# Kernel tuning notes

Hardware: AMD Instinct MI355X
Metric: run time of the kernel (lower is better)

## Reference

```python
import jax, jax.numpy as jnp
import numpy as np

# dims: L layers, D d_model, H heads, DH head_dim, DFF ffn, V vocab, BLK nf4 blocksize
L, D, H, DH, DFF, V, BLK = 2, 2048, 16, 128, 5504, 32000, 64
B, S, C, T = 4, 1000, 7, 45

# bitsandbytes NF4 codebook (fixed 16 quantiles of N(0,1), normalized to [-1,1])
NF4 = jnp.array([-1.0, -0.6961928009986877, -0.5250730514526367, -0.39491748809814453,
                 -0.28444138169288635, -0.18477343022823334, -0.09105003625154495, 0.0,
                 0.07958029955625534, 0.16093020141124725, 0.24611230194568634,
                 0.3379152417182922, 0.44070982933044434, 0.5626170039176941,
                 0.7229568362236023, 1.0], dtype=jnp.float32)


def _dequant(idx, scale):
    # idx: [out, in] int in [0,16); scale: [out, in//BLK] per-block absmax
    o, i = idx.shape
    return (NF4[idx].reshape(o, i // BLK, BLK) * scale[:, :, None]).reshape(o, i)


def _rmsnorm(h, w, eps=1e-5):
    return h * jax.lax.rsqrt(jnp.mean(h * h, axis=-1, keepdims=True) + eps) * w


def _rot_half(x):
    x1, x2 = jnp.split(x, 2, axis=-1)
    return jnp.concatenate([-x2, x1], axis=-1)


def _llama_fwd(token_ids, embed, wq_idx, wq_scale, wk_idx, wk_scale, wv_idx, wv_scale,
               wo_idx, wo_scale, wg_idx, wg_scale, wu_idx, wu_scale, wd_idx, wd_scale,
               ln1_w, ln2_w, lnf_w):
    Bt, St = token_ids.shape
    h = embed[token_ids]  # [B,S,D]
    # rotary embeddings
    inv = 1.0 / (10000.0 ** (jnp.arange(0, DH, 2, dtype=jnp.float32) / DH))
    ang = jnp.arange(St, dtype=jnp.float32)[:, None] * inv[None, :]  # [S, DH/2]
    emb_ang = jnp.concatenate([ang, ang], axis=-1)  # [S, DH]
    cos, sin = jnp.cos(emb_ang), jnp.sin(emb_ang)
    mask = jnp.where(jnp.tril(jnp.ones((St, St), dtype=bool)), 0.0, -1e9)  # causal
    for l in range(L):
        xn = _rmsnorm(h, ln1_w[l])
        q = (xn @ _dequant(wq_idx[l], wq_scale[l]).T).reshape(Bt, St, H, DH).transpose(0, 2, 1, 3)
        k = (xn @ _dequant(wk_idx[l], wk_scale[l]).T).reshape(Bt, St, H, DH).transpose(0, 2, 1, 3)
        v = (xn @ _dequant(wv_idx[l], wv_scale[l]).T).reshape(Bt, St, H, DH).transpose(0, 2, 1, 3)
        q = q * cos + _rot_half(q) * sin
        k = k * cos + _rot_half(k) * sin
        att = jax.nn.softmax(jnp.einsum('bhqd,bhkd->bhqk', q, k) / np.float32(np.sqrt(DH)) + mask, axis=-1)
        ctx = jnp.einsum('bhqk,bhkd->bhqd', att, v).transpose(0, 2, 1, 3).reshape(Bt, St, D)
        h = h + ctx @ _dequant(wo_idx[l], wo_scale[l]).T
        xn = _rmsnorm(h, ln2_w[l])
        g = xn @ _dequant(wg_idx[l], wg_scale[l]).T
        u = xn @ _dequant(wu_idx[l], wu_scale[l]).T
        h = h + (jax.nn.silu(g) * u) @ _dequant(wd_idx[l], wd_scale[l]).T
    # hidden_states[-1].mean(dim=1)
    return _rmsnorm(h, lnf_w).mean(axis=1)


def setup_inputs() -> dict:
    key = jax.random.key(0)
    ks = jax.random.split(key, 20)
    ridx = lambda k, shp: jax.random.randint(k, shp, 0, 16, dtype=jnp.int32)
    rsc = lambda k, shp: jax.random.uniform(k, shp, minval=0.01, maxval=0.03, dtype=jnp.float32)
    return {
        'x': jax.random.normal(ks[0], (B, C, T), dtype=jnp.float32),
        'token_ids': jax.random.randint(ks[1], (B, S), 0, V, dtype=jnp.int32),
        'embed': jax.random.normal(ks[2], (V, D), dtype=jnp.float32) * 0.02,
        'wq_idx': ridx(ks[3], (L, D, D)), 'wq_scale': rsc(ks[4], (L, D, D // BLK)),
        'wk_idx': ridx(ks[5], (L, D, D)), 'wk_scale': rsc(ks[6], (L, D, D // BLK)),
        'wv_idx': ridx(ks[7], (L, D, D)), 'wv_scale': rsc(ks[8], (L, D, D // BLK)),
        'wo_idx': ridx(ks[9], (L, D, D)), 'wo_scale': rsc(ks[10], (L, D, D // BLK)),
        'wg_idx': ridx(ks[11], (L, DFF, D)), 'wg_scale': rsc(ks[12], (L, DFF, D // BLK)),
        'wu_idx': ridx(ks[13], (L, DFF, D)), 'wu_scale': rsc(ks[14], (L, DFF, D // BLK)),
        'wd_idx': ridx(ks[15], (L, D, DFF)), 'wd_scale': rsc(ks[16], (L, D, DFF // BLK)),
        'ln1_w': jnp.ones((L, D), dtype=jnp.float32),
        'ln2_w': jnp.ones((L, D), dtype=jnp.float32),
        'lnf_w': jnp.ones((D,), dtype=jnp.float32),
        'proj_w': jax.random.normal(ks[17], (D, T), dtype=jnp.float32) * 0.05,
        'proj_b': jnp.zeros((D,), dtype=jnp.float32),
    }


def reference(x, token_ids, embed, wq_idx, wq_scale, wk_idx, wk_scale, wv_idx, wv_scale,
              wo_idx, wo_scale, wg_idx, wg_scale, wu_idx, wu_scale, wd_idx, wd_scale,
              ln1_w, ln2_w, lnf_w, proj_w, proj_b):
    # NF4-quantized Llama-style causal LM forward + mean pool over sequence
    e_text = _llama_fwd(token_ids, embed, wq_idx, wq_scale, wk_idx, wk_scale, wv_idx, wv_scale,
                        wo_idx, wo_scale, wg_idx, wg_scale, wu_idx, wu_scale, wd_idx, wd_scale,
                        ln1_w, ln2_w, lnf_w)  # [B, D]
    # series branch: channel-mean -> linear -> L2 normalize
    series_mean = x.mean(axis=1)  # [B, T]
    series_emb = series_mean @ proj_w.T + proj_b  # [B, D]
    series_emb = series_emb / jnp.maximum(jnp.linalg.norm(series_emb, axis=-1, keepdims=True), 1e-12)
    return e_text + series_emb
```

## Files before the change

### kernel.cpp

```cpp
#include <hip/hip_runtime.h>
#include <hip/hip_bf16.h>

#define L_N 2
#define D_ 2048
#define H_ 16
#define DH_ 128
#define DFF_ 5504
#define B_ 4
#define S_ 1000
#define C_ 7
#define T_ 45
#define M_ 4000

typedef short bf16x8 __attribute__((ext_vector_type(8)));
typedef float f32x4 __attribute__((ext_vector_type(4)));

__constant__ float NF4_TAB[16] = {
  -1.0f, -0.6961928009986877f, -0.5250730514526367f, -0.39491748809814453f,
  -0.28444138169288635f, -0.18477343022823334f, -0.09105003625154495f, 0.0f,
  0.07958029955625534f, 0.16093020141124725f, 0.24611230194568634f,
  0.3379152417182922f, 0.44070982933044434f, 0.5626170039176941f,
  0.7229568362236023f, 1.0f };

__device__ __forceinline__ unsigned short f2bf(float f) {
  unsigned int u = __float_as_uint(f);
  u += 0x7fffu + ((u >> 16) & 1u);
  return (unsigned short)(u >> 16);
}
__device__ __forceinline__ float bf2f(unsigned short u) {
  return __uint_as_float(((unsigned int)u) << 16);
}
__device__ __forceinline__ f32x4 zero4() { f32x4 z; z[0]=0.f; z[1]=0.f; z[2]=0.f; z[3]=0.f; return z; }
__device__ __forceinline__ f32x4 mfma16(bf16x8 a, bf16x8 b, f32x4 c) {
  return __builtin_amdgcn_mfma_f32_16x16x32_bf16(a, b, c, 0, 0, 0);
}

typedef __attribute__((address_space(3))) unsigned int lds_u32;
typedef const __attribute__((address_space(1))) unsigned int glb_u32;
__device__ __forceinline__ void gload16(const void* g, void* l) {
  __builtin_amdgcn_global_load_lds((glb_u32*)g, (lds_u32*)l, 16, 0, 0);
}

__global__ void rope_tables(float* __restrict__ cosT, float* __restrict__ sinT) {
  int s = blockIdx.x, d = threadIdx.x;
  int j = d & 63;
  float inv = expf(-(float)j * (9.210340371976184f / 64.f));
  float ang = (float)s * inv;
  cosT[s * DH_ + d] = cosf(ang);
  sinT[s * DH_ + d] = sinf(ang);
}

__global__ __launch_bounds__(256) void embed_gather(const int* __restrict__ tok,
    const float* __restrict__ emb, float* __restrict__ h) {
  int row = blockIdx.x;
  int tk = tok[row];
  const float4* src = reinterpret_cast<const float4*>(emb + (size_t)tk * D_);
  float4* dst = reinterpret_cast<float4*>(h + (size_t)row * D_);
  dst[threadIdx.x] = src[threadIdx.x];
  dst[threadIdx.x + 256] = src[threadIdx.x + 256];
}

__global__ __launch_bounds__(256) void rmsnorm_k(float* __restrict__ h,
    const float* __restrict__ add, const float* __restrict__ w,
    unsigned short* __restrict__ out) {
  const int row = blockIdx.x, t = threadIdx.x;
  float* hp = h + (size_t)row * D_;
  float4 a = *reinterpret_cast<const float4*>(&hp[t * 8]);
  float4 b = *reinterpret_cast<const float4*>(&hp[t * 8 + 4]);
  if (add) {
    const float* ap = add + (size_t)row * D_;
    float4 da = *reinterpret_cast<const float4*>(&ap[t * 8]);
    float4 db = *reinterpret_cast<const float4*>(&ap[t * 8 + 4]);
    a.x += da.x; a.y += da.y; a.z += da.z; a.w += da.w;
    b.x += db.x; b.y += db.y; b.z += db.z; b.w += db.w;
    *reinterpret_cast<float4*>(&hp[t * 8]) = a;
    *reinterpret_cast<float4*>(&hp[t * 8 + 4]) = b;
  }
  float ss = a.x*a.x + a.y*a.y + a.z*a.z + a.w*a.w
           + b.x*b.x + b.y*b.y + b.z*b.z + b.w*b.w;
#pragma unroll
  for (int m = 1; m < 64; m <<= 1) ss += __shfl_xor(ss, m);
  __shared__ float red[4];
  if ((t & 63) == 0) red[t >> 6] = ss;
  __syncthreads();
  float tot = red[0] + red[1] + red[2] + red[3];
  float rs = rsqrtf(tot * (1.0f / D_) + 1e-5f);
  float4 wa = *reinterpret_cast<const float4*>(&w[t * 8]);
  float4 wb = *reinterpret_cast<const float4*>(&w[t * 8 + 4]);
  unsigned r0 = (unsigned)f2bf(a.x*rs*wa.x) | ((unsigned)f2bf(a.y*rs*wa.y) << 16);
  unsigned r1 = (unsigned)f2bf(a.z*rs*wa.z) | ((unsigned)f2bf(a.w*rs*wa.w) << 16);
  unsigned r2 = (unsigned)f2bf(b.x*rs*wb.x) | ((unsigned)f2bf(b.y*rs*wb.y) << 16);
  unsigned r3 = (unsigned)f2bf(b.z*rs*wb.z) | ((unsigned)f2bf(b.w*rs*wb.w) << 16);
  int4 ov; ov.x = (int)r0; ov.y = (int)r1; ov.z = (int)r2; ov.w = (int)r3;
  *reinterpret_cast<int4*>(&out[(size_t)row * D_ + t * 8]) = ov;
}

struct DqJob { const int* idx; const float* sc; unsigned short* out; };
struct DqBatch { DqJob j[4]; };

__global__ __launch_bounds__(256) void dequant_batch(DqBatch bt, int K) {
  __shared__ float nf4[16];
  const int t = threadIdx.x;
  if (t < 16) nf4[t] = NF4_TAB[t];
  __syncthreads();
  const DqJob jb = bt.j[blockIdx.z];
  const int row = blockIdx.y;
  const int k0 = blockIdx.x * 2048 + t * 8;
  if (k0 >= K) return;
  const size_t base = (size_t)row * K + k0;
  int4 a = *reinterpret_cast<const int4*>(&jb.idx[base]);
  int4 b = *reinterpret_cast<const int4*>(&jb.idx[base + 4]);
  float s = jb.sc[(size_t)row * (K >> 6) + (k0 >> 6)];
  unsigned r0 = (unsigned)f2bf(nf4[a.x & 15] * s) | ((unsigned)f2bf(nf4[a.y & 15] * s) << 16);
  unsigned r1 = (unsigned)f2bf(nf4[a.z & 15] * s) | ((unsigned)f2bf(nf4[a.w & 15] * s) << 16);
  unsigned r2 = (unsigned)f2bf(nf4[b.x & 15] * s) | ((unsigned)f2bf(nf4[b.y & 15] * s) << 16);
  unsigned r3 = (unsigned)f2bf(nf4[b.z & 15] * s) | ((unsigned)f2bf(nf4[b.w & 15] * s) << 16);
  int4 ov; ov.x = (int)r0; ov.y = (int)r1; ov.z = (int)r2; ov.w = (int)r3;
  *reinterpret_cast<int4*>(&jb.out[base]) = ov;
}

template<int MODE>
__global__ __launch_bounds__(256, 4) void gemm_bf16(
    const unsigned short* __restrict__ A,
    const unsigned short* __restrict__ Bw,
    const unsigned short* __restrict__ Bw2,
    int Mdim, int N, int K, int nx, int ksplit,
    void* outp, void* outp2, float* dscr) {
  __shared__ unsigned short A_lds[128 * 64];
  __shared__ unsigned short B_lds[128 * 64];
  const int t = threadIdx.x;
  const int lane = t & 63, wid = t >> 6;
  const int z = blockIdx.z;

  const unsigned short* Bsrc = (MODE == 0 && z) ? Bw2 : Bw;
  void* osel = (MODE == 0 && z) ? outp2 : outp;

  const int bid = blockIdx.x;
  const int xcd = bid & 7, l = bid >> 3;
  const int m_blk = xcd * 4 + (l & 3);
  const int n_blk = l >> 2;
  const int n0 = n_blk * 128;
  const int m0 = m_blk * 128;

  const int wm = (wid >> 1) * 64, wn = (wid & 1) * 64;
  const int lr = lane & 15, lg = lane >> 4;
  const int lrow = lane >> 3;
  const int lslot = (((lane & 7) ^ lrow) << 4);
  const int rswz = (lr & 7) << 4;

  f32x4 acc[4][4];
#pragma unroll
  for (int i = 0; i < 4; ++i)
#pragma unroll
    for (int j = 0; j < 4; ++j) acc[i][j] = zero4();

  const int kT = K >> 6;
  const int ktlo = (MODE == 3) ? (z ? ksplit : 0) : 0;
  const int kthi = (MODE == 3) ? (z ? kT : ksplit) : kT;
  const size_t rowb = (size_t)(K * 2);

  for (int kt = ktlo; kt < kthi; ++kt) {
#pragma unroll
    for (int c0 = 0; c0 < 4; ++c0) {
      const int c = wid + 4 * c0;
      int gr = m0 + c * 8 + lrow;
      gr = gr < Mdim ? gr : Mdim - 1;
      gload16((const char*)A + (size_t)gr * rowb + kt * 128 + lslot,
              (char*)&A_lds[0] + c * 1024);
      const int nr = n0 + c * 8 + lrow;
      gload16((const char*)Bsrc + (size_t)nr * rowb + kt * 128 + lslot,
              (char*)&B_lds[0] + c * 1024);
    }
    __syncthreads();
#pragma unroll
    for (int ks = 0; ks < 2; ++ks) {
      bf16x8 af[4], bfr[4];
      const int cb = (ks * 64 + lg * 16) ^ rswz;
#pragma unroll
      for (int i = 0; i < 4; ++i) {
        af[i]  = *reinterpret_cast<const bf16x8*>(
                   (const char*)&A_lds[0] + (wm + i * 16 + lr) * 128 + cb);
        bfr[i] = *reinterpret_cast<const bf16x8*>(
                   (const char*)&B_lds[0] + (wn + i * 16 + lr) * 128 + cb);
      }
      __builtin_amdgcn_s_setprio(1);
#pragma unroll
      for (int mi = 0; mi < 4; ++mi)
#pragma unroll
        for (int ni = 0; ni < 4; ++ni)
          acc[mi][ni] = mfma16(af[mi], bfr[ni], acc[mi][ni]);
      __builtin_amdgcn_s_setprio(0);
    }
    __syncthreads();
  }

#pragma unroll
  for (int mi = 0; mi < 4; ++mi) {
#pragma unroll
    for (int r = 0; r < 4; ++r) {
      int gm = m0 + wm + mi * 16 + lg * 4 + r;
      if (gm >= Mdim) continue;
#pragma unroll
      for (int ni = 0; ni < 4; ++ni) {
        int gn = n0 + wn + ni * 16 + lr;
        float v = acc[mi][ni][r];
        if (MODE == 0) {
          ((unsigned short*)osel)[(size_t)gm * N + gn] = f2bf(v);
        } else if (MODE == 1) {
          const int which = gn >> 11;
          const int hh = (gn >> 7) & 15, dd = gn & 127;
          const int b = gm / S_, s = gm - b * S_;
          ((unsigned short*)outp)[
            (((size_t)which * (B_ * H_) + b * H_ + hh) * S_ + s) * DH_ + dd] = f2bf(v);
        } else {
          if (z == 0) ((float*)outp)[(size_t)gm * N + gn] += v;
          else        dscr[(size_t)gm * N + gn] = v;
        }
      }
    }
  }
}

__global__ __launch_bounds__(256) void silu_mul(unsigned short* __restrict__ g,
    const unsigned short* __restrict__ u) {
  const size_t i = ((size_t)blockIdx.x * 256 + threadIdx.x) * 8;
  int4 gv = *reinterpret_cast<const int4*>(&g[i]);
  int4 uv = *reinterpret_cast<const int4*>(&u[i]);
  const unsigned* gp = reinterpret_cast<const unsigned*>(&gv);
  const unsigned* up = reinterpret_cast<const unsigned*>(&uv);
  unsigned ov[4];
#pragma unroll
  for (int j = 0; j < 4; ++j) {
    float g0 = bf2f(gp[j] & 0xffffu), g1 = bf2f(gp[j] >> 16);
    float u0 = bf2f(up[j] & 0xffffu), u1 = bf2f(up[j] >> 16);
    float s0 = g0 / (1.f + __expf(-g0)) * u0;
    float s1 = g1 / (1.f + __expf(-g1)) * u1;
    ov[j] = (unsigned)f2bf(s0) | ((unsigned)f2bf(s1) << 16);
  }
  int4 o; o.x = (int)ov[0]; o.y = (int)ov[1]; o.z = (int)ov[2]; o.w = (int)ov[3];
  *reinterpret_cast<int4*>(&g[i]) = o;
}

__global__ __launch_bounds__(256) void rope_apply(unsigned short* __restrict__ qb,
    unsigned short* __restrict__ kb, const float* __restrict__ cosT,
    const float* __restrict__ sinT) {
  size_t i = (size_t)blockIdx.x * 256 + threadIdx.x;
  int d = (int)(i & 63);
  size_t row = i >> 6;
  int s = (int)(row % S_);
  size_t base = row * DH_;
  float c = cosT[s * DH_ + d], sn = sinT[s * DH_ + d];
  float q0 = bf2f(qb[base + d]), q1 = bf2f(qb[base + d + 64]);
  qb[base + d]      = f2bf(q0 * c - q1 * sn);
  qb[base + d + 64] = f2bf(q1 * c + q0 * sn);
  float k0 = bf2f(kb[base + d]), k1 = bf2f(kb[base + d + 64]);
  kb[base + d]      = f2bf(k0 * c - k1 * sn);
  kb[base + d + 64] = f2bf(k1 * c + k0 * sn);
}

__global__ __launch_bounds__(256) void vtrans_k(const unsigned short* __restrict__ vb,
    unsigned short* __restrict__ vt) {
  __shared__ unsigned int tile[64][33];
  const int t = threadIdx.x;
  const int s0 = blockIdx.x * 64, d0 = blockIdx.y * 64, bh = blockIdx.z;
#pragma unroll
  for (int j = 0; j < 2; ++j) {
    int idx = t + 256 * j;
    int s_r = idx >> 3, c8 = (idx & 7) << 3;
    int srow = s0 + s_r; srow = srow < S_ ? srow : S_ - 1;
    int4 v = *reinterpret_cast<const int4*>(&vb[((size_t)bh * S_ + srow) * DH_ + d0 + c8]);
    tile[s_r][(c8 >> 1) + 0] = (unsigned)v.x;
    tile[s_r][(c8 >> 1) + 1] = (unsigned)v.y;
    tile[s_r][(c8 >> 1) + 2] = (unsigned)v.z;
    tile[s_r][(c8 >> 1) + 3] = (unsigned)v.w;
  }
  __syncthreads();
#pragma unroll
  for (int j = 0; j < 2; ++j) {
    int idx = t + 256 * j;
    int d_r = idx >> 3, s8 = (idx & 7) << 3;
    unsigned r[8];
#pragma unroll
    for (int e = 0; e < 8; ++e) {
      unsigned wv = tile[s8 + e][d_r >> 1];
      r[e] = (d_r & 1) ? (wv >> 16) : (wv & 0xffffu);
    }
    int4 ov;
    ov.x = (int)(r[0] | (r[1] << 16));
    ov.y = (int)(r[2] | (r[3] << 16));
    ov.z = (int)(r[4] | (r[5] << 16));
    ov.w = (int)(r[6] | (r[7] << 16));
    *reinterpret_cast<int4*>(&vt[((size_t)(bh * 128 + d0 + d_r)) * 1024 + s0 + s8]) = ov;
  }
}

__global__ __launch_bounds__(512, 4) void attn2_k(const unsigned short* __restrict__ qg,
    const unsigned short* __restrict__ kg, const unsigned short* __restrict__ vtg,
    unsigned short* __restrict__ ctx) {
  __shared__ unsigned short K_lds[64 * 128];
  __shared__ unsigned short VT_lds[128 * 64];
  const int t = threadIdx.x, lane = t & 63, w = t >> 6;
  const int lr = lane & 15, lg = lane >> 4;
  const int bh = blockIdx.x, qt = blockIdx.y;
  const int q0 = qt * 128;
  const int b = bh >> 4, hh = bh & 15;
  const size_t kbase2 = (size_t)bh * S_ * DH_ * 2;
  const int q_idx = q0 + w * 16 + lr;
  const int swz = (lr & 7) << 4;

  bf16x8 qf[4];
#pragma unroll
  for (int ks = 0; ks < 4; ++ks) {
    bf16x8 z;
#pragma unroll
    for (int e = 0; e < 8; ++e) z[e] = 0;
    if (q_idx < S_)
      z = *reinterpret_cast<const bf16x8*>(
            (const char*)qg + kbase2 + (size_t)q_idx * 256 + ks * 64 + lg * 16);
    qf[ks] = z;
  }
  float mst = -1e30f, lst = 0.f;
  f32x4 cacc[8];
#pragma unroll
  for (int f = 0; f < 8; ++f) cacc[f] = zero4();

  const int q_hi = (q0 + 127 < S_) ? q0 + 127 : S_ - 1;
  const int nt = q_hi / 64 + 1;
  const int wq_max = q0 + w * 16 + 15;

  for (int kt = 0; kt < nt; ++kt) {
    const int kv0 = kt * 64;
    __syncthreads();
#pragma unroll
    for (int j = 0; j < 2; ++j) {
      const int chunk = w + 8 * j;
      int krow = chunk * 4 + (lane >> 4);
      int kcolb = (lane & 15) << 4;
      int gr = kv0 + krow; gr = gr < S_ ? gr : S_ - 1;
      gload16((const char*)kg + kbase2 + (size_t)gr * 256 + (kcolb ^ ((krow & 7) << 4)),
              (char*)K_lds + chunk * 1024);
      int vrow = chunk * 8 + (lane >> 3);
      int vcolb = (lane & 7) << 4;
      gload16((const char*)vtg + ((size_t)(bh * 128 + vrow) * 1024 + kv0) * 2 + (vcolb ^ ((vrow & 7) << 4)),
              (char*)VT_lds + chunk * 1024);
    }
    __syncthreads();
    if (kv0 > wq_max) continue;

    f32x4 sacc[4];
#pragma unroll
    for (int c = 0; c < 4; ++c) sacc[c] = zero4();
#pragma unroll
    for (int ks = 0; ks < 4; ++ks) {
#pragma unroll
      for (int c = 0; c < 4; ++c) {
        bf16x8 kf = *reinterpret_cast<const bf16x8*>(
            &K_lds[(c * 16 + lr) * 128 + (((ks * 64 + lg * 16) ^ swz) >> 1)]);
        sacc[c] = mfma16(kf, qf[ks], sacc[c]);
      }
    }
    float p[4][4];
    float mx = -1e30f;
#pragma unroll
    for (int c = 0; c < 4; ++c)
#pragma unroll
      for (int r = 0; r < 4; ++r) {
        int kv = kv0 + c * 16 + lg * 4 + r;
        float v = sacc[c][r] * 0.08838834764831845f;
        if (kv > q_idx || kv >= S_) v = -1e30f;
        p[c][r] = v;
        mx = fmaxf(mx, v);
      }
    mx = fmaxf(mx, __shfl_xor(mx, 16));
    mx = fmaxf(mx, __shfl_xor(mx, 32));
    float mn = fmaxf(mst, mx);
    float corr = __expf(mst - mn);
    mst = mn;
    float rs = 0.f;
#pragma unroll
    for (int c = 0; c < 4; ++c)
#pragma unroll
      for (int r = 0; r < 4; ++r) {
        float e = __expf(p[c][r] - mn);
        p[c][r] = e;
        rs += e;
      }
    rs += __shfl_xor(rs, 16);
    rs += __shfl_xor(rs, 32);
    lst = lst * corr + rs;
#pragma unroll
    for (int f = 0; f < 8; ++f)
#pragma unroll
      for (int r = 0; r < 4; ++r) cacc[f][r] *= corr;

    unsigned pk01[4], pk23[4];
#pragma unroll
    for (int c = 0; c < 4; ++c) {
      pk01[c] = (unsigned)f2bf(p[c][0]) | ((unsigned)f2bf(p[c][1]) << 16);
      pk23[c] = (unsigned)f2bf(p[c][2]) | ((unsigned)f2bf(p[c][3]) << 16);
    }
#pragma unroll
    for (int ks = 0; ks < 2; ++ks) {
      unsigned bu[4];
#pragma unroll
      for (int jj = 0; jj < 4; ++jj) {
        const int srcl = ((lg & 1) * 2 + (jj >> 1)) * 16 + lr;
        unsigned lo = (unsigned)__shfl((int)((jj & 1) ? pk23[2 * ks]     : pk01[2 * ks]),     srcl);
        unsigned hi = (unsigned)__shfl((int)((jj & 1) ? pk23[2 * ks + 1] : pk01[2 * ks + 1]), srcl);
        bu[jj] = (lg >= 2) ? hi : lo;
      }
      union { unsigned u[4]; bf16x8 v; } pb;
      pb.u[0] = bu[0]; pb.u[1] = bu[1]; pb.u[2] = bu[2]; pb.u[3] = bu[3];
#pragma unroll
      for (int f = 0; f < 8; ++f) {
        bf16x8 vtf = *reinterpret_cast<const bf16x8*>(
            &VT_lds[(f * 16 + lr) * 64 + (((ks * 64 + lg * 16) ^ swz) >> 1)]);
        cacc[f] = mfma16(vtf, pb.v, cacc[f]);
      }
    }
  }

  if (q_idx < S_) {
    float inv = 1.f / lst;
    unsigned short* cp = ctx + ((size_t)(b * S_ + q_idx)) * D_ + hh * 128;
#pragma unroll
    for (int f = 0; f < 8; ++f) {
      unsigned lo = (unsigned)f2bf(cacc[f][0] * inv) | ((unsigned)f2bf(cacc[f][1] * inv) << 16);
      unsigned hi = (unsigned)f2bf(cacc[f][2] * inv) | ((unsigned)f2bf(cacc[f][3] * inv) << 16);
      uint2 ov; ov.x = lo; ov.y = hi;
      *reinterpret_cast<uint2*>(cp + f * 16 + lg * 4) = ov;
    }
  }
}

__global__ __launch_bounds__(256) void meanpool(const unsigned short* __restrict__ xn,
    float* __restrict__ out) {
  int d = blockIdx.x * 256 + threadIdx.x;
  int b = blockIdx.y;
  const unsigned short* p = xn + (size_t)b * S_ * D_ + d;
  float s = 0.f;
  for (int i = 0; i < S_; ++i) s += bf2f(p[(size_t)i * D_]);
  out[(size_t)b * D_ + d] = s * (1.f / S_);
}

__global__ __launch_bounds__(256) void series_k(const float* __restrict__ x,
    const float* __restrict__ pw, const float* __restrict__ pb, float* out) {
  __shared__ float sm[T_];
  __shared__ float emb[D_];
  __shared__ float red[4];
  int b = blockIdx.x, t = threadIdx.x;
  if (t < T_) {
    float s = 0.f;
    for (int c = 0; c < C_; ++c) s += x[((size_t)b * C_ + c) * T_ + t];
    sm[t] = s * (1.f / C_);
  }
  __syncthreads();
  float ssq = 0.f;
#pragma unroll
  for (int j = 0; j < D_ / 256; ++j) {
    int d = j * 256 + t;
    float e = pb[d];
    for (int tt = 0; tt < T_; ++tt) e += sm[tt] * pw[(size_t)d * T_ + tt];
    emb[d] = e;
    ssq += e * e;
  }
#pragma unroll
  for (int m = 1; m < 64; m <<= 1) ssq += __shfl_xor(ssq, m);
  if ((t & 63) == 0) red[t >> 6] = ssq;
  __syncthreads();
  float tot = red[0] + red[1] + red[2] + red[3];
  float inv = 1.f / fmaxf(sqrtf(tot), 1e-12f);
#pragma unroll
  for (int j = 0; j < D_ / 256; ++j) {
    int d = j * 256 + t;
    out[(size_t)b * D_ + d] += emb[d] * inv;
  }
}

extern "C" void kernel_launch(void* const* d_in, const int* in_sizes, int n_in,
                              void* d_out, int out_size, void* d_ws, size_t ws_size,
                              hipStream_t stream) {
  const float* x      = (const float*)d_in[0];
  const int*   tok    = (const int*)d_in[1];
  const float* embedw = (const float*)d_in[2];
  const int*   wq_idx = (const int*)d_in[3];
  const float* wq_sc  = (const float*)d_in[4];
  const int*   wk_idx = (const int*)d_in[5];
  const float* wk_sc  = (const float*)d_in[6];
  const int*   wv_idx = (const int*)d_in[7];
  const float* wv_sc  = (const float*)d_in[8];
  const int*   wo_idx = (const int*)d_in[9];
  const float* wo_sc  = (const float*)d_in[10];
  const int*   wg_idx = (const int*)d_in[11];
  const float* wg_sc  = (const float*)d_in[12];
  const int*   wu_idx = (const int*)d_in[13];
  const float* wu_sc  = (const float*)d_in[14];
  const int*   wd_idx = (const int*)d_in[15];
  const float* wd_sc  = (const float*)d_in[16];
  const float* ln1    = (const float*)d_in[17];
  const float* ln2    = (const float*)d_in[18];
  const float* lnf    = (const float*)d_in[19];
  const float* projw  = (const float*)d_in[20];
  const float* projb  = (const float*)d_in[21];
  float* out = (float*)d_out;
  (void)in_sizes; (void)n_in; (void)out_size; (void)ws_size;

  char* wsp = (char*)d_ws;
  size_t off = 0;
  auto alloc = [&](size_t bytes) -> void* {
    void* p = wsp + off; off += (bytes + 255) & ~(size_t)255; return p; };
  float* cosT = (float*)alloc((size_t)S_ * DH_ * 4);
  float* sinT = (float*)alloc((size_t)S_ * DH_ * 4);
  float* hbuf = (float*)alloc((size_t)M_ * D_ * 4);
  unsigned short* xn   = (unsigned short*)alloc((size_t)M_ * D_ * 2);
  unsigned short* qkv  = (unsigned short*)alloc((size_t)3 * B_ * H_ * S_ * DH_ * 2);
  unsigned short* wdeq = (unsigned short*)alloc((size_t)2 * DFF_ * D_ * 2);
  unsigned short* vt   = (unsigned short*)alloc((size_t)B_ * H_ * DH_ * 1024 * 2);
  void* R = alloc((size_t)M_ * DFF_ * 2);
  float* dscr = (float*)R;
  unsigned short* ubuf = (unsigned short*)R;
  const size_t NH = (size_t)B_ * H_ * S_ * DH_;
  unsigned short* qb = qkv, *kb = qkv + NH, *vb = qkv + 2 * NH;
  unsigned short* ctx  = xn;
  unsigned short* gbuf = qkv;

  rope_tables<<<S_, DH_, 0, stream>>>(cosT, sinT);
  embed_gather<<<M_, 256, 0, stream>>>(tok, embedw, hbuf);

  const int my = (M_ + 127) / 128;
  const dim3 gQKV((3 * D_ / 128) * my);
  const dim3 gAtt((D_ / 128) * my, 1, 2);
  const dim3 gMlp((DFF_ / 128) * my, 1, 2);
  const size_t DD = (size_t)D_ * D_;
  const size_t FD = (size_t)DFF_ * D_;

  for (int l = 0; l < L_N; ++l) {
    const int*   wqi = wq_idx + (size_t)l * DD;
    const float* wqs = wq_sc + (size_t)l * D_ * (D_ / 64);
    const int*   wki = wk_idx + (size_t)l * DD;
    const float* wks = wk_sc + (size_t)l * D_ * (D_ / 64);
    const int*   wvi = wv_idx + (size_t)l * DD;
    const float* wvs = wv_sc + (size_t)l * D_ * (D_ / 64);
    const int*   woi = wo_idx + (size_t)l * DD;
    const float* wos = wo_sc + (size_t)l * D_ * (D_ / 64);
    const int*   wgi = wg_idx + (size_t)l * FD;
    const float* wgs = wg_sc + (size_t)l * DFF_ * (D_ / 64);
    const int*   wui = wu_idx + (size_t)l * FD;
    const float* wus = wu_sc + (size_t)l * DFF_ * (D_ / 64);
    const int*   wdi = wd_idx + (size_t)l * FD;
    const float* wds = wd_sc + (size_t)l * D_ * (DFF_ / 64);

    rmsnorm_k<<<M_, 256, 0, stream>>>(hbuf, l == 0 ? nullptr : dscr, ln1 + l * D_, xn);

    {
      DqBatch bt;
      bt.j[0] = { wqi, wqs, wdeq };
      bt.j[1] = { wki, wks, wdeq + DD };
      bt.j[2] = { wvi, wvs, wdeq + 2 * DD };
      bt.j[3] = { woi, wos, wdeq + 3 * DD };
      dequant_batch<<<dim3(1, D_, 4), 256, 0, stream>>>(bt, D_);
    }
    gemm_bf16<1><<<gQKV, 256, 0, stream>>>(xn, wdeq, nullptr, M_, 3 * D_, D_,
                                           3 * D_ / 128, 0, qkv, nullptr, nullptr);
    rope_apply<<<(B_ * H_ * S_ * 64) / 256, 256, 0, stream>>>(qb, kb, cosT, sinT);
    vtrans_k<<<dim3(16, 2, B_ * H_), 256, 0, stream>>>(vb, vt);
    attn2_k<<<dim3(B_ * H_, 8), 512, 0, stream>>>(qb, kb, vt, ctx);
    gemm_bf16<3><<<gAtt, 256, 0, stream>>>(ctx, wdeq + 3 * DD, nullptr, M_, D_, D_,
                                           D_ / 128, 16, hbuf, nullptr, dscr);
    rmsnorm_k<<<M_, 256, 0, stream>>>(hbuf, dscr, ln2 + l * D_, xn);

    {
      DqBatch bt;
      bt.j[0] = { wgi, wgs, wdeq };
      bt.j[1] = { wui, wus, wdeq + FD };
      bt.j[2] = bt.j[0]; bt.j[3] = bt.j[0];
      dequant_batch<<<dim3(1, DFF_, 2), 256, 0, stream>>>(bt, D_);
    }
    gemm_bf16<0><<<gMlp, 256, 0, stream>>>(xn, wdeq, wdeq + FD, M_, DFF_, D_,
                                           DFF_ / 128, 0, gbuf, ubuf, nullptr);
    silu_mul<<<(M_ * DFF_ / 8) / 256, 256, 0, stream>>>(gbuf, ubuf);

    {
      DqBatch bt;
      bt.j[0] = { wdi, wds, wdeq };
      bt.j[1] = bt.j[0]; bt.j[2] = bt.j[0]; bt.j[3] = bt.j[0];
      dequant_batch<<<dim3(3, D_, 1), 256, 0, stream>>>(bt, DFF_);
    }
    gemm_bf16<3><<<gAtt, 256, 0, stream>>>(gbuf, wdeq, nullptr, M_, D_, DFF_,
                                           D_ / 128, 43, hbuf, nullptr, dscr);
  }

  rmsnorm_k<<<M_, 256, 0, stream>>>(hbuf, dscr, lnf, xn);
  meanpool<<<dim3(D_ / 256, B_), 256, 0, stream>>>(xn, out);
  series_k<<<B_, 256, 0, stream>>>(x, projw, projb, out);
}
```

Before: 1.308 ms.

## Add double-buffered LDS GEMM for QKV and gate/up projections

Introduces a gemm_pipe kernel that double-buffers the A and B tiles in LDS, issuing global-to-LDS loads for the next K-tile before computing the current one and waiting with a partial vmcnt. It also raises wave priority around the MFMA block. The QKV and MLP gate/up GEMMs switch to it, aiming to hide global memory latency behind matrix math. LDS use doubles to 64KB per block, which may lower occupancy below the requested launch bound.

```diff
diff --git a/kernel.cpp b/kernel.cpp
--- a/kernel.cpp
+++ b/kernel.cpp
@@ -117,6 +117,115 @@
   unsigned r3 = (unsigned)f2bf(nf4[b.z & 15] * s) | ((unsigned)f2bf(nf4[b.w & 15] * s) << 16);
   int4 ov; ov.x = (int)r0; ov.y = (int)r1; ov.z = (int)r2; ov.w = (int)r3;
   *reinterpret_cast<int4*>(&jb.out[base]) = ov;
+}
+
+template<int MODE>
+__global__ __launch_bounds__(256, 4) void gemm_pipe(
+    const unsigned short* __restrict__ A,
+    const unsigned short* __restrict__ Bw,
+    const unsigned short* __restrict__ Bw2,
+    int Mdim, int N, int K,
+    void* outp, void* outp2) {
+  __shared__ unsigned short A_lds[2][128 * 64];
+  __shared__ unsigned short B_lds[2][128 * 64];
+  const int t = threadIdx.x;
+  const int lane = t & 63, wid = t >> 6;
+  const int z = blockIdx.z;
+
+  const unsigned short* Bsrc = (MODE == 0 && z) ? Bw2 : Bw;
+  void* osel = (MODE == 0 && z) ? outp2 : outp;
+
+  const int bid = blockIdx.x;
+  const int xcd = bid & 7, l = bid >> 3;
+  const int m_blk = xcd * 4 + (l & 3);
+  const int n_blk = l >> 2;
+  const int n0 = n_blk * 128;
+  const int m0 = m_blk * 128;
+
+  const int wm = (wid >> 1) * 64, wn = (wid & 1) * 64;
+  const int lr = lane & 15, lg = lane >> 4;
+  const int lrow = lane >> 3;
+  const int lslot = (((lane & 7) ^ lrow) << 4);
+  const int rswz = (lr & 7) << 4;
+
+  f32x4 acc[4][4];
+#pragma unroll
+  for (int i = 0; i < 4; ++i)
+#pragma unroll
+    for (int j = 0; j < 4; ++j) acc[i][j] = zero4();
+
+  const int kT = K >> 6;
+  const size_t rowb = (size_t)(K * 2);
+
+  auto stage = [&](int kt, int b) {
+#pragma unroll
+    for (int c0 = 0; c0 < 4; ++c0) {
+      const int c = wid + 4 * c0;
+      int gr = m0 + c * 8 + lrow;
+      gr = gr < Mdim ? gr : Mdim - 1;
+      gload16((const char*)A + (size_t)gr * rowb + kt * 128 + lslot,
+              (char*)&A_lds[b][0] + c * 1024);
+      const int nr = n0 + c * 8 + lrow;
+      gload16((const char*)Bsrc + (size_t)nr * rowb + kt * 128 + lslot,
+              (char*)&B_lds[b][0] + c * 1024);
+    }
+  };
+
+  stage(0, 0);
+  for (int kt = 0; kt < kT; ++kt) {
+    const int cur = kt & 1;
+    if (kt + 1 < kT) {
+      stage(kt + 1, cur ^ 1);
+      asm volatile("s_waitcnt vmcnt(8)" ::: "memory");
+    } else {
+      asm volatile("s_waitcnt vmcnt(0)" ::: "memory");
+    }
+    __builtin_amdgcn_s_barrier();
+    __builtin_amdgcn_sched_barrier(0);
+#pragma unroll
+    for (int ks = 0; ks < 2; ++ks) {
+      bf16x8 af[4], bfr[4];
+      const int cb = (ks * 64 + lg * 16) ^ rswz;
+#pragma unroll
+      for (int i = 0; i < 4; ++i) {
+        af[i]  = *reinterpret_cast<const bf16x8*>(
+                   (const char*)&A_lds[cur][0] + (wm + i * 16 + lr) * 128 + cb);
+        bfr[i] = *reinterpret_cast<const bf16x8*>(
+                   (const char*)&B_lds[cur][0] + (wn + i * 16 + lr) * 128 + cb);
+      }
+      __builtin_amdgcn_s_setprio(1);
+#pragma unroll
+      for (int mi = 0; mi < 4; ++mi)
+#pragma unroll
+        for (int ni = 0; ni < 4; ++ni)
+          acc[mi][ni] = mfma16(af[mi], bfr[ni], acc[mi][ni]);
+      __builtin_amdgcn_s_setprio(0);
+    }
+    __builtin_amdgcn_s_barrier();
+  }
+
+#pragma unroll
+  for (int mi = 0; mi < 4; ++mi) {
+#pragma unroll
+    for (int r = 0; r < 4; ++r) {
+      int gm = m0 + wm + mi * 16 + lg * 4 + r;
+      if (gm >= Mdim) continue;
+#pragma unroll
+      for (int ni = 0; ni < 4; ++ni) {
+        int gn = n0 + wn + ni * 16 + lr;
+        float v = acc[mi][ni][r];
+        if (MODE == 0) {
+          ((unsigned short*)osel)[(size_t)gm * N + gn] = f2bf(v);
+        } else {
+          const int which = gn >> 11;
+          const int hh = (gn >> 7) & 15, dd = gn & 127;
+          const int b = gm / S_, s = gm - b * S_;
+          ((unsigned short*)outp)[
+            (((size_t)which * (B_ * H_) + b * H_ + hh) * S_ + s) * DH_ + dd] = f2bf(v);
+        }
+      }
+    }
+  }
 }
 
 template<int MODE>
@@ -560,8 +669,8 @@
       bt.j[3] = { woi, wos, wdeq + 3 * DD };
       dequant_batch<<<dim3(1, D_, 4), 256, 0, stream>>>(bt, D_);
     }
-    gemm_bf16<1><<<gQKV, 256, 0, stream>>>(xn, wdeq, nullptr, M_, 3 * D_, D_,
-                                           3 * D_ / 128, 0, qkv, nullptr, nullptr);
+    gemm_pipe<1><<<gQKV, 256, 0, stream>>>(xn, wdeq, nullptr, M_, 3 * D_, D_,
+                                           qkv, nullptr);
     rope_apply<<<(B_ * H_ * S_ * 64) / 256, 256, 0, stream>>>(qb, kb, cosT, sinT);
     vtrans_k<<<dim3(16, 2, B_ * H_), 256, 0, stream>>>(vb, vt);
     attn2_k<<<dim3(B_ * H_, 8), 512, 0, stream>>>(qb, kb, vt, ctx);
@@ -576,8 +685,8 @@
       bt.j[2] = bt.j[0]; bt.j[3] = bt.j[0];
       dequant_batch<<<dim3(1, DFF_, 2), 256, 0, stream>>>(bt, D_);
     }
-    gemm_bf16<0><<<gMlp, 256, 0, stream>>>(xn, wdeq, wdeq + FD, M_, DFF_, D_,
-                                           DFF_ / 128, 0, gbuf, ubuf, nullptr);
+    gemm_pipe<0><<<gMlp, 256, 0, stream>>>(xn, wdeq, wdeq + FD, M_, DFF_, D_,
+                                           gbuf, ubuf);
     silu_mul<<<(M_ * DFF_ / 8) / 256, 256, 0, stream>>>(gbuf, ubuf);
 
     {
```

New measurement: 1.425 ms. +9.0%, slower.
